# Optimization experiments

Hardware: AMD Instinct MI355X
Metric: run time of the kernel (lower is better)

The kernel has to match this reference:

```python
import jax, jax.numpy as jnp
import numpy as np

D_MODEL = 256
N_LEVELS = 4
N_HEADS = 8
N_POINTS = 4
LEN_Q = 1024
LEN_X = 256
SHAPES_NP = np.array([[100, 100], [50, 50], [25, 25], [13, 13]], dtype=np.int32)
LEN_IN = int((SHAPES_NP[:, 0] * SHAPES_NP[:, 1]).sum())  # 13294


def setup_inputs() -> dict:
    key = jax.random.key(0)
    ks = jax.random.split(key, 10)
    s = 0.02
    lvl_start = np.concatenate([[0], np.cumsum(SHAPES_NP[:, 0] * SHAPES_NP[:, 1])[:-1]]).astype(np.int32)
    return {
        "query": jax.random.normal(ks[0], (1, LEN_Q, D_MODEL), jnp.float32),
        "reference_points": jax.random.uniform(ks[1], (1, LEN_Q, N_LEVELS, 2), jnp.float32),
        "input_flatten": jax.random.normal(ks[2], (1, LEN_IN, D_MODEL), jnp.float32),
        "input_spatial_shapes": jnp.asarray(SHAPES_NP, jnp.int32),
        "add_keys": jax.random.normal(ks[3], (1, LEN_X, D_MODEL), jnp.float32),
        "input_level_start_index": jnp.asarray(lvl_start, jnp.int32),
        "W_off": jax.random.normal(ks[4], (N_HEADS * N_LEVELS * N_POINTS * 2, D_MODEL), jnp.float32) * s,
        "b_off": jax.random.normal(ks[5], (N_HEADS * N_LEVELS * N_POINTS * 2,), jnp.float32),
        "W_attn": jax.random.normal(ks[6], (N_HEADS * (N_LEVELS + 1), D_MODEL, D_MODEL), jnp.float32) * s,
        "W_val": jax.random.normal(ks[7], (2 * N_HEADS, D_MODEL, D_MODEL), jnp.float32) * s,
        "b_val": jax.random.normal(ks[8], (2 * N_HEADS, D_MODEL), jnp.float32) * s,
        "W_mix": jax.random.normal(ks[9], (D_MODEL, N_HEADS + 1), jnp.float32) * s,
    }


def reference(query, reference_points, input_flatten, input_spatial_shapes, add_keys,
              input_level_start_index, W_off, b_off, W_attn, W_val, b_val, W_mix):
    N, Lq, C = query.shape
    H, L, P = N_HEADS, N_LEVELS, N_POINTS

    # sampling offsets: (N, Lq, H, L, P, 2)
    off = (query @ W_off.T + b_off).reshape(N, Lq, H, L, P, 2)
    iss_f = input_spatial_shapes.astype(jnp.float32)          # (L, 2) = (H_l, W_l)
    wh = iss_f[:, ::-1]                                        # (W_l, H_l)
    loc = reference_points[:, :, None, :, None, :] + off / wh[None, None, None, :, None, :]

    # get_keys: clamp, quantize to int index (matches torch .int() trunc, values >= 0)
    loc = jnp.clip(loc, 0.0, 0.999)
    idx = (loc * iss_f[None, None, None, :, None, :]).astype(jnp.int32)
    h_l = input_spatial_shapes[:, 0]                           # (L,)
    flat_idx = (idx[..., 0] + idx[..., 1] * h_l[None, None, None, :, None]
                + input_level_start_index[None, None, None, :, None])   # (N, Lq, H, L, P)
    keys = input_flatten[0][flat_idx[0]]                       # (Lq, H, L, P, C)
    keys = jnp.transpose(keys, (1, 2, 3, 0, 4))                # (H, L, P, Lq, C)

    q = query.reshape(Lq, C)
    head_w = jax.nn.softmax(W_mix.T, axis=0)                   # (H+1, C), softmax over heads
    result = q * head_w[-1][None]
    addk = add_keys.reshape(-1, C)                             # (Lx, C)

    for h in range(H):
        attn = []
        for lvl in range(L):
            simil = W_attn[h * L + lvl]
            # faithful to torch: (C, P*Lq) row-major reshaped to (P, Lq, C)
            ki = (simil @ keys[h, lvl].reshape(-1, C).T).reshape(P, Lq, C)
            attn.append((ki * q[None]).sum(-1))                # (P, Lq)
        simil = W_attn[h * L + L]
        ki = addk @ simil.T                                    # (Lx, C)
        attn.append(ki @ q.T)                                  # (Lx, Lq)
        attn = jax.nn.softmax(jnp.concatenate(attn, axis=0), axis=0)  # (L*P+Lx, Lq)

        vals = (keys[h].reshape(-1, C) @ W_val[2 * h].T + b_val[2 * h]).reshape(L * P, Lq, C)
        v2 = addk @ W_val[2 * h + 1].T + b_val[2 * h + 1]      # (Lx, C)
        vals = jnp.concatenate([vals, jnp.broadcast_to(v2[:, None], (v2.shape[0], Lq, C))], axis=0)
        result = result + (attn[:, :, None] * vals).sum(0) * head_w[h][None]

    return result[None]
```

## Files before the change

### kernel.cpp

```cpp
#include <hip/hip_runtime.h>

typedef unsigned short ushort_t;
typedef __attribute__((ext_vector_type(8))) short bh8;
typedef __attribute__((ext_vector_type(4))) float f4;
typedef __attribute__((ext_vector_type(4))) unsigned int u4;

__device__ __forceinline__ ushort_t f2bf(float f) {
  unsigned u = __float_as_uint(f);
  return (ushort_t)((u + 0x7FFFu + ((u >> 16) & 1u)) >> 16);
}
__device__ __forceinline__ float bf2f(ushort_t v) {
  return __uint_as_float(((unsigned)v) << 16);
}

template <typename OutT>
__device__ __forceinline__ void gemm_abt_core(
    char* smem,
    const ushort_t* __restrict__ A, const ushort_t* __restrict__ B,
    OutT* __restrict__ C, int ldA, int ldB, int ldC, int K, int m0, int n0)
{
  ushort_t* As = (ushort_t*)smem;
  ushort_t* Bs = (ushort_t*)(smem + 10240);
  int t = threadIdx.x;
  int lane = t & 63, w = t >> 6;
  int quad = lane >> 4, l15 = lane & 15;
  int wm = w >> 1, wn = w & 1;
  f4 acc[4][4];
  #pragma unroll
  for (int mi = 0; mi < 4; ++mi)
    #pragma unroll
    for (int ni = 0; ni < 4; ++ni) acc[mi][ni] = (f4)0.f;
  int row = t >> 1, kh = (t & 1) * 16;
  const ushort_t* pa = A + (m0 + row) * ldA + kh;
  const ushort_t* pb = B + (n0 + row) * ldB + kh;
  u4 va0 = *(const u4*)(pa);     u4 va1 = *(const u4*)(pa + 8);
  u4 vb0 = *(const u4*)(pb);     u4 vb1 = *(const u4*)(pb + 8);
  for (int k0 = 0; k0 < K; k0 += 32) {
    if (k0) __syncthreads();
    {
      u4* da = (u4*)(As + row * 40 + kh); da[0] = va0; da[1] = va1;
      u4* db = (u4*)(Bs + row * 40 + kh); db[0] = vb0; db[1] = vb1;
    }
    if (k0 + 32 < K) {
      va0 = *(const u4*)(pa + k0 + 32); va1 = *(const u4*)(pa + k0 + 40);
      vb0 = *(const u4*)(pb + k0 + 32); vb1 = *(const u4*)(pb + k0 + 40);
    }
    __syncthreads();
    bh8 af[4], bfv[4];
    #pragma unroll
    for (int mi = 0; mi < 4; ++mi)
      af[mi] = *(bh8*)(As + (wm * 64 + mi * 16 + l15) * 40 + quad * 8);
    #pragma unroll
    for (int ni = 0; ni < 4; ++ni)
      bfv[ni] = *(bh8*)(Bs + (wn * 64 + ni * 16 + l15) * 40 + quad * 8);
    #pragma unroll
    for (int mi = 0; mi < 4; ++mi)
      #pragma unroll
      for (int ni = 0; ni < 4; ++ni)
        acc[mi][ni] = __builtin_amdgcn_mfma_f32_16x16x32_bf16(af[mi], bfv[ni], acc[mi][ni], 0, 0, 0);
  }
  #pragma unroll
  for (int mi = 0; mi < 4; ++mi)
    #pragma unroll
    for (int ni = 0; ni < 4; ++ni)
      #pragma unroll
      for (int r = 0; r < 4; ++r) {
        int mg = m0 + wm * 64 + mi * 16 + quad * 4 + r;
        int ng = n0 + wn * 64 + ni * 16 + l15;
        if constexpr (sizeof(OutT) == 4) C[mg * ldC + ng] = acc[mi][ni][r];
        else C[mg * ldC + ng] = (OutT)f2bf(acc[mi][ni][r]);
      }
}

__device__ __forceinline__ void gemm_abt_12864(
    char* smem,
    const ushort_t* __restrict__ A, const ushort_t* __restrict__ B,
    float* __restrict__ C, int ldA, int ldB, int ldC, int K, int m0, int n0)
{
  ushort_t* As = (ushort_t*)smem;
  ushort_t* Bs = (ushort_t*)(smem + 10240);
  int t = threadIdx.x;
  int lane = t & 63, w = t >> 6;
  int quad = lane >> 4, l15 = lane & 15;
  int wm = w >> 1, wn = w & 1;
  f4 acc[4][2];
  #pragma unroll
  for (int mi = 0; mi < 4; ++mi)
    #pragma unroll
    for (int ni = 0; ni < 2; ++ni) acc[mi][ni] = (f4)0.f;
  int rowA = t >> 1, khA = (t & 1) * 16;
  int rowB = t >> 2, khB = (t & 3) * 8;
  const ushort_t* pa = A + (m0 + rowA) * ldA + khA;
  const ushort_t* pb = B + (n0 + rowB) * ldB + khB;
  u4 va0 = *(const u4*)(pa); u4 va1 = *(const u4*)(pa + 8);
  u4 vb0 = *(const u4*)(pb);
  for (int k0 = 0; k0 < K; k0 += 32) {
    if (k0) __syncthreads();
    {
      u4* da = (u4*)(As + rowA * 40 + khA); da[0] = va0; da[1] = va1;
      u4* db = (u4*)(Bs + rowB * 40 + khB); db[0] = vb0;
    }
    if (k0 + 32 < K) {
      va0 = *(const u4*)(pa + k0 + 32); va1 = *(const u4*)(pa + k0 + 40);
      vb0 = *(const u4*)(pb + k0 + 32);
    }
    __syncthreads();
    bh8 af[4], bf2[2];
    #pragma unroll
    for (int mi = 0; mi < 4; ++mi)
      af[mi] = *(bh8*)(As + (wm * 64 + mi * 16 + l15) * 40 + quad * 8);
    #pragma unroll
    for (int ni = 0; ni < 2; ++ni)
      bf2[ni] = *(bh8*)(Bs + (wn * 32 + ni * 16 + l15) * 40 + quad * 8);
    #pragma unroll
    for (int mi = 0; mi < 4; ++mi)
      #pragma unroll
      for (int ni = 0; ni < 2; ++ni)
        acc[mi][ni] = __builtin_amdgcn_mfma_f32_16x16x32_bf16(af[mi], bf2[ni], acc[mi][ni], 0, 0, 0);
  }
  #pragma unroll
  for (int mi = 0; mi < 4; ++mi)
    #pragma unroll
    for (int ni = 0; ni < 2; ++ni)
      #pragma unroll
      for (int r = 0; r < 4; ++r) {
        int mg = m0 + wm * 64 + mi * 16 + quad * 4 + r;
        int ng = n0 + wn * 32 + ni * 16 + l15;
        C[mg * ldC + ng] = acc[mi][ni][r];
      }
}

__device__ __forceinline__ void gemm_abt_f32in(
    char* smem,
    const float* __restrict__ A, const float* __restrict__ B,
    ushort_t* __restrict__ C, int ldA, int ldB, int ldC, int K, int m0, int n0)
{
  ushort_t* As = (ushort_t*)smem;
  ushort_t* Bs = (ushort_t*)(smem + 10240);
  int t = threadIdx.x;
  int lane = t & 63, w = t >> 6;
  int quad = lane >> 4, l15 = lane & 15;
  int wm = w >> 1, wn = w & 1;
  f4 acc[4][4];
  #pragma unroll
  for (int mi = 0; mi < 4; ++mi)
    #pragma unroll
    for (int ni = 0; ni < 4; ++ni) acc[mi][ni] = (f4)0.f;
  int row = t >> 1, kh = (t & 1) * 16;
  const float* pa = A + (m0 + row) * ldA + kh;
  const float* pb = B + (n0 + row) * ldB + kh;
  float4 fa[4], fb[4];
  #pragma unroll
  for (int i = 0; i < 4; ++i) {
    fa[i] = *(const float4*)(pa + i * 4);
    fb[i] = *(const float4*)(pb + i * 4);
  }
  for (int k0 = 0; k0 < K; k0 += 32) {
    if (k0) __syncthreads();
    {
      ushort_t* da = As + row * 40 + kh;
      ushort_t* db = Bs + row * 40 + kh;
      #pragma unroll
      for (int i = 0; i < 4; ++i) {
        ushort4 oa; oa.x = f2bf(fa[i].x); oa.y = f2bf(fa[i].y);
        oa.z = f2bf(fa[i].z); oa.w = f2bf(fa[i].w);
        *(ushort4*)(da + i * 4) = oa;
        ushort4 ob; ob.x = f2bf(fb[i].x); ob.y = f2bf(fb[i].y);
        ob.z = f2bf(fb[i].z); ob.w = f2bf(fb[i].w);
        *(ushort4*)(db + i * 4) = ob;
      }
    }
    if (k0 + 32 < K) {
      #pragma unroll
      for (int i = 0; i < 4; ++i) {
        fa[i] = *(const float4*)(pa + k0 + 32 + i * 4);
        fb[i] = *(const float4*)(pb + k0 + 32 + i * 4);
      }
    }
    __syncthreads();
    bh8 af[4], bfv[4];
    #pragma unroll
    for (int mi = 0; mi < 4; ++mi)
      af[mi] = *(bh8*)(As + (wm * 64 + mi * 16 + l15) * 40 + quad * 8);
    #pragma unroll
    for (int ni = 0; ni < 4; ++ni)
      bfv[ni] = *(bh8*)(Bs + (wn * 64 + ni * 16 + l15) * 40 + quad * 8);
    #pragma unroll
    for (int mi = 0; mi < 4; ++mi)
      #pragma unroll
      for (int ni = 0; ni < 4; ++ni)
        acc[mi][ni] = __builtin_amdgcn_mfma_f32_16x16x32_bf16(af[mi], bfv[ni], acc[mi][ni], 0, 0, 0);
  }
  #pragma unroll
  for (int mi = 0; mi < 4; ++mi)
    #pragma unroll
    for (int ni = 0; ni < 4; ++ni)
      #pragma unroll
      for (int r = 0; r < 4; ++r) {
        int mg = m0 + wm * 64 + mi * 16 + quad * 4 + r;
        int ng = n0 + wn * 64 + ni * 16 + l15;
        C[mg * ldC + ng] = (ushort_t)f2bf(acc[mi][ni][r]);
      }
}

__global__ __launch_bounds__(256) void k_fused_cast_off(
    const float* __restrict__ q, const float* __restrict__ xin,
    const float* __restrict__ addk, const float* __restrict__ Wval,
    const float* __restrict__ Wattn, ushort_t* __restrict__ arena,
    const float* __restrict__ Woff, const float* __restrict__ boff,
    const float* __restrict__ refpts, const int* __restrict__ shapes,
    const int* __restrict__ lvlst, int* __restrict__ fidx,
    ushort_t* __restrict__ tmp)
{
  __shared__ __align__(16) char smem[20480];
  if (blockIdx.x >= 96) {
    const int total4 = 1719168;
    for (int i = (blockIdx.x - 96) * 256 + threadIdx.x; i < total4; i += 1952 * 256) {
      const float* src; ushort_t* dst; int e;
      if (i < 65536)        { src = q    + i * 4;            dst = arena + i * 4; }
      else if (i < 916352)  { e = i - 65536;  src = xin  + e * 4; dst = arena + 262144  + e * 4; }
      else if (i < 932736)  { e = i - 916352; src = addk + e * 4; dst = arena + 3665408 + e * 4; }
      else if (i < 1194880) {
        e = i - 932736; int el = e * 4;
        int h = el >> 17, r = el & 131071;
        int c = r >> 9, k = r & 511;
        src = Wval + (2 * h + (k >> 8)) * 65536 + c * 256 + (k & 255);
        dst = arena + 3730944 + el;
      }
      else {
        e = i - 1194880;
        src = Wattn + e * 4;
        dst = arena + 6352384 + e * 4;
      }
      float4 v = *(const float4*)src;
      ushort4 o; o.x = f2bf(v.x); o.y = f2bf(v.y); o.z = f2bf(v.z); o.w = f2bf(v.w);
      *(ushort4*)dst = o;
    }
  } else if (blockIdx.x >= 64) {
    int e = blockIdx.x - 64;
    int h = e >> 2, rem = e & 3, my = rem >> 1, nx = rem & 1;
    gemm_abt_f32in(smem, addk, Wattn + (h * 4 + 4) * 65536, tmp + h * 65536,
                   256, 256, 256, 256, my * 128, nx * 128);
  } else {
    float(*As)[65] = (float(*)[65])smem;
    float(*Bs)[65] = (float(*)[65])(smem + 16 * 65 * 4);
    int e = blockIdx.x;
    int nx = e & 3, my = e >> 2;
    int m0 = my * 64, n0 = nx * 64;
    int t = threadIdx.x;
    int tm = t & 15, tn = t >> 4;
    int lr = t >> 4, lc = t & 15;
    float acc[4][4] = {};
    float qa[4], wb[4];
    #pragma unroll
    for (int i = 0; i < 4; ++i) {
      int r = lr + i * 16;
      qa[i] = q[(m0 + r) * 256 + lc];
      wb[i] = Woff[(n0 + r) * 256 + lc];
    }
    for (int k0 = 0; k0 < 256; k0 += 16) {
      if (k0) __syncthreads();
      #pragma unroll
      for (int i = 0; i < 4; ++i) {
        int r = lr + i * 16;
        As[lc][r] = qa[i];
        Bs[lc][r] = wb[i];
      }
      if (k0 + 16 < 256) {
        #pragma unroll
        for (int i = 0; i < 4; ++i) {
          int r = lr + i * 16;
          qa[i] = q[(m0 + r) * 256 + k0 + 16 + lc];
          wb[i] = Woff[(n0 + r) * 256 + k0 + 16 + lc];
        }
      }
      __syncthreads();
      #pragma unroll
      for (int k = 0; k < 16; ++k) {
        float a[4], b[4];
        #pragma unroll
        for (int i = 0; i < 4; ++i) a[i] = As[k][tm * 4 + i];
        #pragma unroll
        for (int j = 0; j < 4; ++j) b[j] = Bs[k][tn * 4 + j];
        #pragma unroll
        for (int i = 0; i < 4; ++i)
          #pragma unroll
          for (int j = 0; j < 4; ++j) acc[i][j] += a[i] * b[j];
      }
    }
    #pragma unroll
    for (int i = 0; i < 4; ++i) {
      int b = m0 + tm * 4 + i;
      #pragma unroll
      for (int jp = 0; jp < 2; ++jp) {
        int tt = ((n0 + tn * 4) >> 1) + jp;
        int l = (tt >> 2) & 3;
        float off0 = acc[i][jp * 2]     + boff[2 * tt];
        float off1 = acc[i][jp * 2 + 1] + boff[2 * tt + 1];
        int Hi = shapes[2 * l], Wi = shapes[2 * l + 1];
        float Hf = (float)Hi, Wf = (float)Wi;
        float r0 = refpts[b * 8 + 2 * l], r1 = refpts[b * 8 + 2 * l + 1];
        float l0 = fminf(fmaxf(r0 + off0 / Wf, 0.f), 0.999f);
        float l1 = fminf(fmaxf(r1 + off1 / Hf, 0.f), 0.999f);
        int i0 = (int)(l0 * Hf);
        int i1 = (int)(l1 * Wf);
        fidx[b * 128 + tt] = i0 + i1 * Hi + lvlst[l];
      }
    }
  }
}

__device__ __forceinline__ void attn_mfma_body(
    char* smemc,
    const ushort_t* __restrict__ qbf, const ushort_t* __restrict__ xbf,
    const ushort_t* __restrict__ Wlvl, const int* __restrict__ fidx,
    float* __restrict__ attnP, int bx)
{
  unsigned* Bs0 = (unsigned*)smemc;
  unsigned* Bs1 = (unsigned*)(smemc + 8704);
  ushort_t* As0 = (ushort_t*)(smemc + 17408);
  ushort_t* As1 = (ushort_t*)(smemc + 26624);
  int* fis = (int*)(smemc + 35840);
  float* Nlds = (float*)smemc;

  int h = bx >> 8, l = (bx >> 6) & 3, g = bx & 63;
  int ch = g & 3, g2 = g >> 2;
  int p = g2 >> 2, tg = g2 & 3;
  int c0 = ch * 64;
  int t = threadIdx.x;
  int lane = t & 63, w = t >> 6;
  int quad = lane >> 4, l15 = lane & 15;
  int qcol = p * 4 + tg;
  fis[t] = fidx[(tg * 256 + t) * 128 + h * 16 + l * 4 + p];
  __syncthreads();
  f4 acc[4];
  #pragma unroll
  for (int mi = 0; mi < 4; ++mi) acc[mi] = (f4)0.f;

  int cl = t & 63, sg = t >> 6;
  int uu = t >> 2, jj0 = (t & 3) * 16;
  const ushort_t* qrow = qbf + (uu * 16 + qcol) * 256 + jj0;

  unsigned vv[16];
  u4 a0, a1;
  #pragma unroll
  for (int rr = 0; rr < 16; ++rr)
    vv[rr] = xbf[fis[sg * 16 + rr] * 256 + c0 + cl];
  { const u4* src = (const u4*)qrow; a0 = src[0]; a1 = src[1]; }
  #pragma unroll
  for (int i = 0; i < 4; ++i) {
    uint2 w2; w2.x = vv[i * 4] | (vv[i * 4 + 1] << 16);
    w2.y = vv[i * 4 + 2] | (vv[i * 4 + 3] << 16);
    *(uint2*)&Bs0[cl * 34 + sg * 8 + i * 2] = w2;
  }
  { u4* dst = (u4*)(As0 + uu * 72 + jj0); dst[0] = a0; dst[1] = a1; }
  #pragma unroll
  for (int rr = 0; rr < 16; ++rr)
    vv[rr] = xbf[fis[64 + sg * 16 + rr] * 256 + c0 + cl];
  { const u4* src = (const u4*)(qrow + 64); a0 = src[0]; a1 = src[1]; }
  __syncthreads();

  #pragma unroll
  for (int jt = 0; jt < 4; ++jt) {
    unsigned* Bc = (jt & 1) ? Bs1 : Bs0;
    ushort_t* Ac = (jt & 1) ? As1 : As0;
    if (jt < 3) {
      unsigned* Bn = (jt & 1) ? Bs0 : Bs1;
      ushort_t* An = (jt & 1) ? As0 : As1;
      #pragma unroll
      for (int i = 0; i < 4; ++i) {
        uint2 w2; w2.x = vv[i * 4] | (vv[i * 4 + 1] << 16);
        w2.y = vv[i * 4 + 2] | (vv[i * 4 + 3] << 16);
        *(uint2*)&Bn[cl * 34 + sg * 8 + i * 2] = w2;
      }
      { u4* dst = (u4*)(An + uu * 72 + jj0); dst[0] = a0; dst[1] = a1; }
      if (jt < 2) {
        #pragma unroll
        for (int rr = 0; rr < 16; ++rr)
          vv[rr] = xbf[fis[(jt + 2) * 64 + sg * 16 + rr] * 256 + c0 + cl];
        const u4* src = (const u4*)(qrow + (jt + 2) * 64);
        a0 = src[0]; a1 = src[1];
      }
    }
    #pragma unroll
    for (int ks = 0; ks < 2; ++ks) {
      bh8 af[4], bfv;
      #pragma unroll
      for (int mi = 0; mi < 4; ++mi)
        af[mi] = *(bh8*)(Ac + (mi * 16 + l15) * 72 + ks * 32 + quad * 8);
      {
        const unsigned* bp = &Bc[(w * 16 + l15) * 34 + ks * 16 + quad * 4];
        uint2 b0 = *(const uint2*)bp;
        uint2 b1 = *(const uint2*)(bp + 2);
        u4 bb; bb.x = b0.x; bb.y = b0.y; bb.z = b1.x; bb.w = b1.y;
        bfv = __builtin_bit_cast(bh8, bb);
      }
      #pragma unroll
      for (int mi = 0; mi < 4; ++mi)
        acc[mi] = __builtin_amdgcn_mfma_f32_16x16x32_bf16(af[mi], bfv, acc[mi], 0, 0, 0);
    }
    if (jt < 3) __syncthreads();
  }
  __syncthreads();
  #pragma unroll
  for (int mi = 0; mi < 4; ++mi)
    *(f4*)&Nlds[(w * 16 + l15) * 68 + mi * 16 + quad * 4] = acc[mi];
  __syncthreads();
  {
    int a = t >> 6, u = t & 63;
    const ushort_t* Wr = Wlvl + (h * 4 + l) * 65536 + (a * 64 + u) * 256 + c0;
    float s = 0.f;
    #pragma unroll
    for (int cc = 0; cc < 8; ++cc) {
      u4 wv = *(const u4*)(Wr + cc * 8);
      int cb = cc * 8;
      s += __uint_as_float(wv.x << 16)         * Nlds[(cb + 0) * 68 + u];
      s += __uint_as_float(wv.x & 0xffff0000u) * Nlds[(cb + 1) * 68 + u];
      s += __uint_as_float(wv.y << 16)         * Nlds[(cb + 2) * 68 + u];
      s += __uint_as_float(wv.y & 0xffff0000u) * Nlds[(cb + 3) * 68 + u];
      s += __uint_as_float(wv.z << 16)         * Nlds[(cb + 4) * 68 + u];
      s += __uint_as_float(wv.z & 0xffff0000u) * Nlds[(cb + 5) * 68 + u];
      s += __uint_as_float(wv.w << 16)         * Nlds[(cb + 6) * 68 + u];
      s += __uint_as_float(wv.w & 0xffff0000u) * Nlds[(cb + 7) * 68 + u];
    }
    attnP[ch * 131072 + (h * 16 + l * 4 + a) * 1024 + u * 16 + qcol] = s;
  }
}

__global__ __launch_bounds__(256, 4) void k_fused_attn(
    const ushort_t* __restrict__ qbf, const ushort_t* __restrict__ xbf,
    const ushort_t* __restrict__ Wlvl, const int* __restrict__ fidx,
    float* __restrict__ attnP,
    const ushort_t* __restrict__ tmp, float* __restrict__ attn)
{
  __shared__ __align__(16) char smem[36864];
  int bx = blockIdx.x;
  if (bx >= 256) {
    attn_mfma_body(smem, qbf, xbf, Wlvl, fidx, attnP, bx - 256);
  } else {
    int e = bx;
    int h = e >> 5, rem = e & 31, my = rem >> 4, nx = rem & 15;
    gemm_abt_12864(smem, tmp + h * 65536, qbf, attn + h * 278528 + 16384,
                   256, 256, 1024, 256, my * 128, nx * 64);
  }
}

__global__ __launch_bounds__(256) void k_softmax(
    float* __restrict__ attn, const float* __restrict__ attnP,
    ushort_t* __restrict__ attn2bf, float* __restrict__ s1, float* __restrict__ s2)
{
  __shared__ float red[16][17];
  int h = blockIdx.y;
  int bl = threadIdx.x & 15;
  int b = blockIdx.x * 16 + bl;
  int rg = threadIdx.x >> 4;
  const int R0 = rg * 17;
  float* col = attn + h * 278528 + b;
  float v[17];
  float m = -1e30f;
  #pragma unroll
  for (int i = 0; i < 17; ++i) {
    int r = R0 + i;
    float x;
    if (r < 16) {
      int idx = (h * 16 + r) * 1024 + b;
      x = attnP[idx] + attnP[131072 + idx] + attnP[262144 + idx] + attnP[393216 + idx];
    } else {
      x = col[r * 1024];
    }
    v[i] = x;
    m = fmaxf(m, x);
  }
  red[rg][bl] = m;
  __syncthreads();
  #pragma unroll
  for (int j = 0; j < 16; ++j) m = fmaxf(m, red[j][bl]);
  float sum = 0.f;
  #pragma unroll
  for (int i = 0; i < 17; ++i) { v[i] = expf(v[i] - m); sum += v[i]; }
  __syncthreads();
  red[rg][bl] = sum;
  __syncthreads();
  float tot = 0.f;
  #pragma unroll
  for (int j = 0; j < 16; ++j) tot += red[j][bl];
  float inv = 1.f / tot;
  #pragma unroll
  for (int i = 0; i < 17; ++i) {
    int r = R0 + i;
    float x = v[i] * inv;
    if (r < 16) col[r * 1024] = x;
    else attn2bf[h * 262144 + (r - 16) * 1024 + b] = f2bf(x);
  }
  if (rg == 0) {
    float sa = 0.f;
    #pragma unroll
    for (int i = 0; i < 16; ++i) sa += v[i];
    float sn = sa * inv;
    s1[h * 1024 + b] = sn;
    s2[h * 1024 + b] = 1.f - sn;
  }
}

__global__ __launch_bounds__(256) void k_fused_kbar_tn(
    const ushort_t* __restrict__ xbf, const float* __restrict__ attn,
    const int* __restrict__ fidx, const ushort_t* __restrict__ attn2,
    const ushort_t* __restrict__ addk, ushort_t* __restrict__ kabar)
{
  __shared__ __align__(16) unsigned Asu[128 * 20];
  __shared__ __align__(16) unsigned Bsu[128 * 20];
  if (blockIdx.x >= 128) {
    int bb = blockIdx.x - 128;
    int h = bb >> 7, b0 = (bb & 127) * 8;
    int t = threadIdx.x;
    int qi = t >> 5, oct = t & 31;
    int b = b0 + qi;
    float aw[16]; int rowv[16];
    #pragma unroll
    for (int r = 0; r < 16; ++r) {
      aw[r]   = attn[(h * 272 + r) * 1024 + b];
      rowv[r] = fidx[b * 128 + h * 16 + r];
    }
    u4 va[8], vb[8];
    #pragma unroll
    for (int r = 0; r < 8; ++r) va[r] = *(const u4*)(xbf + rowv[r] * 256 + oct * 8);
    #pragma unroll
    for (int r = 0; r < 8; ++r) vb[r] = *(const u4*)(xbf + rowv[8 + r] * 256 + oct * 8);
    float sacc[8] = {};
    #pragma unroll
    for (int r = 0; r < 8; ++r) {
      u4 v = va[r]; float w = aw[r];
      sacc[0] += w * __uint_as_float(v.x << 16);
      sacc[1] += w * __uint_as_float(v.x & 0xffff0000u);
      sacc[2] += w * __uint_as_float(v.y << 16);
      sacc[3] += w * __uint_as_float(v.y & 0xffff0000u);
      sacc[4] += w * __uint_as_float(v.z << 16);
      sacc[5] += w * __uint_as_float(v.z & 0xffff0000u);
      sacc[6] += w * __uint_as_float(v.w << 16);
      sacc[7] += w * __uint_as_float(v.w & 0xffff0000u);
    }
    #pragma unroll
    for (int r = 0; r < 8; ++r) {
      u4 v = vb[r]; float w = aw[8 + r];
      sacc[0] += w * __uint_as_float(v.x << 16);
      sacc[1] += w * __uint_as_float(v.x & 0xffff0000u);
      sacc[2] += w * __uint_as_float(v.y << 16);
      sacc[3] += w * __uint_as_float(v.y & 0xffff0000u);
      sacc[4] += w * __uint_as_float(v.z << 16);
      sacc[5] += w * __uint_as_float(v.z & 0xffff0000u);
      sacc[6] += w * __uint_as_float(v.w << 16);
      sacc[7] += w * __uint_as_float(v.w & 0xffff0000u);
    }
    u4 o;
    o.x = (unsigned)f2bf(sacc[0]) | ((unsigned)f2bf(sacc[1]) << 16);
    o.y = (unsigned)f2bf(sacc[2]) | ((unsigned)f2bf(sacc[3]) << 16);
    o.z = (unsigned)f2bf(sacc[4]) | ((unsigned)f2bf(sacc[5]) << 16);
    o.w = (unsigned)f2bf(sacc[6]) | ((unsigned)f2bf(sacc[7]) << 16);
    *(u4*)(kabar + (h * 1024 + b) * 512 + oct * 8) = o;
  } else {
    int e = blockIdx.x;
    int h = e >> 4, rem = e & 15, my = rem >> 1, nx = rem & 1;
    const ushort_t* A = attn2 + h * 262144;
    const ushort_t* B = addk;
    ushort_t* C = kabar + h * 524288;
    int m0 = my * 128, n0 = nx * 128;
    int t = threadIdx.x;
    int lane = t & 63, w = t >> 6;
    int quad = lane >> 4, l15 = lane & 15;
    int wm = w >> 1, wn = w & 1;
    f4 acc[4][4];
    #pragma unroll
    for (int mi = 0; mi < 4; ++mi)
      #pragma unroll
      for (int ni = 0; ni < 4; ++ni) acc[mi][ni] = (f4)0.f;
    int col = t & 127, half = t >> 7;
    unsigned pa[8], pb[8];
    #pragma unroll
    for (int i = 0; i < 4; ++i) {
      int kpp = half * 4 + i, kk = kpp * 4;
      unsigned x0 = A[(kk + 0) * 1024 + m0 + col], x1 = A[(kk + 1) * 1024 + m0 + col];
      unsigned x2 = A[(kk + 2) * 1024 + m0 + col], x3 = A[(kk + 3) * 1024 + m0 + col];
      pa[i * 2] = x0 | (x1 << 16); pa[i * 2 + 1] = x2 | (x3 << 16);
      unsigned y0 = B[(kk + 0) * 256 + n0 + col], y1 = B[(kk + 1) * 256 + n0 + col];
      unsigned y2 = B[(kk + 2) * 256 + n0 + col], y3 = B[(kk + 3) * 256 + n0 + col];
      pb[i * 2] = y0 | (y1 << 16); pb[i * 2 + 1] = y2 | (y3 << 16);
    }
    for (int k0 = 0; k0 < 256; k0 += 32) {
      if (k0) __syncthreads();
      #pragma unroll
      for (int i = 0; i < 4; ++i) {
        int kpp = half * 4 + i;
        uint2 va; va.x = pa[i * 2]; va.y = pa[i * 2 + 1];
        *(uint2*)&Asu[col * 20 + kpp * 2] = va;
        uint2 vbv; vbv.x = pb[i * 2]; vbv.y = pb[i * 2 + 1];
        *(uint2*)&Bsu[col * 20 + kpp * 2] = vbv;
      }
      if (k0 + 32 < 256) {
        #pragma unroll
        for (int i = 0; i < 4; ++i) {
          int kpp = half * 4 + i, kk = k0 + 32 + kpp * 4;
          unsigned x0 = A[(kk + 0) * 1024 + m0 + col], x1 = A[(kk + 1) * 1024 + m0 + col];
          unsigned x2 = A[(kk + 2) * 1024 + m0 + col], x3 = A[(kk + 3) * 1024 + m0 + col];
          pa[i * 2] = x0 | (x1 << 16); pa[i * 2 + 1] = x2 | (x3 << 16);
          unsigned y0 = B[(kk + 0) * 256 + n0 + col], y1 = B[(kk + 1) * 256 + n0 + col];
          unsigned y2 = B[(kk + 2) * 256 + n0 + col], y3 = B[(kk + 3) * 256 + n0 + col];
          pb[i * 2] = y0 | (y1 << 16); pb[i * 2 + 1] = y2 | (y3 << 16);
        }
      }
      __syncthreads();
      bh8 af[4], bfv[4];
      #pragma unroll
      for (int mi = 0; mi < 4; ++mi)
        af[mi] = *(bh8*)((const ushort_t*)Asu + (wm * 64 + mi * 16 + l15) * 40 + quad * 8);
      #pragma unroll
      for (int ni = 0; ni < 4; ++ni)
        bfv[ni] = *(bh8*)((const ushort_t*)Bsu + (wn * 64 + ni * 16 + l15) * 40 + quad * 8);
      #pragma unroll
      for (int mi = 0; mi < 4; ++mi)
        #pragma unroll
        for (int ni = 0; ni < 4; ++ni)
          acc[mi][ni] = __builtin_amdgcn_mfma_f32_16x16x32_bf16(af[mi], bfv[ni], acc[mi][ni], 0, 0, 0);
    }
    #pragma unroll
    for (int mi = 0; mi < 4; ++mi)
      #pragma unroll
      for (int ni = 0; ni < 4; ++ni)
        #pragma unroll
        for (int r = 0; r < 4; ++r) {
          int mg = m0 + wm * 64 + mi * 16 + quad * 4 + r;
          int ng = n0 + wn * 64 + ni * 16 + l15;
          C[mg * 512 + 256 + ng] = f2bf(acc[mi][ni][r]);
        }
  }
}

__global__ __launch_bounds__(256) void gemm_val_k(
    const ushort_t* __restrict__ kabar, const ushort_t* __restrict__ Wcat,
    float* __restrict__ Y)
{
  __shared__ __align__(16) char smem[20480];
  int h = blockIdx.z;
  gemm_abt_core<float>(smem, kabar + h * 524288, Wcat + h * 131072, Y + h * 262144,
                       512, 512, 256, 512, blockIdx.y * 128, blockIdx.x * 128);
}

__global__ __launch_bounds__(256) void k_combine(
    const float* __restrict__ q, const float* __restrict__ Wmix,
    const float* __restrict__ Y,
    const float* __restrict__ s1, const float* __restrict__ s2,
    const float* __restrict__ bval, float* __restrict__ out)
{
  int b = blockIdx.x, c = threadIdx.x;
  float w[9];
  float m = -1e30f;
  #pragma unroll
  for (int j = 0; j < 9; ++j) { w[j] = Wmix[c * 9 + j]; m = fmaxf(m, w[j]); }
  float tot = 0.f;
  #pragma unroll
  for (int j = 0; j < 9; ++j) { w[j] = expf(w[j] - m); tot += w[j]; }
  float inv = 1.f / tot;
  float res = q[b * 256 + c] * w[8] * inv;
  #pragma unroll
  for (int hh = 0; hh < 8; ++hh) {
    float y = Y[(hh * 1024 + b) * 256 + c]
            + s1[hh * 1024 + b] * bval[(2 * hh) * 256 + c]
            + s2[hh * 1024 + b] * bval[(2 * hh + 1) * 256 + c];
    res += w[hh] * inv * y;
  }
  out[b * 256 + c] = res;
}

extern "C" void kernel_launch(void* const* d_in, const int* in_sizes, int n_in,
                              void* d_out, int out_size, void* d_ws, size_t ws_size,
                              hipStream_t stream) {
  (void)in_sizes; (void)n_in; (void)out_size; (void)ws_size;
  const float* q      = (const float*)d_in[0];
  const float* refpts = (const float*)d_in[1];
  const float* xin    = (const float*)d_in[2];
  const int*   shapes = (const int*)d_in[3];
  const float* addk   = (const float*)d_in[4];
  const int*   lvlst  = (const int*)d_in[5];
  const float* Woff   = (const float*)d_in[6];
  const float* boff   = (const float*)d_in[7];
  const float* Wattn  = (const float*)d_in[8];
  const float* Wval   = (const float*)d_in[9];
  const float* bval   = (const float*)d_in[10];
  const float* Wmix   = (const float*)d_in[11];
  float* out = (float*)d_out;
  float* ws  = (float*)d_ws;

  int*   fidx    = (int*)ws;
  float* s1      = ws + 393216;
  float* s2      = ws + 401408;
  float* attn    = ws + 409600;
  float* Y       = ws + 409600;
  ushort_t* arena = (ushort_t*)(ws + 2637824);
  ushort_t* q_bf     = arena;
  ushort_t* xin_bf   = arena + 262144;
  ushort_t* addk_bf  = arena + 3665408;
  ushort_t* Wcat_bf  = arena + 3730944;
  ushort_t* Wlvl_bf  = arena + 6352384;
  ushort_t* tmp_bf   = arena + 8449536;
  ushort_t* attn2_bf = arena + 8973824;
  ushort_t* kabar_bf = arena + 11070976;
  float* attnP = (float*)(arena + 15265280);

  k_fused_cast_off<<<2048, 256, 0, stream>>>(q, xin, addk, Wval, Wattn, arena,
                                             Woff, boff, refpts, shapes, lvlst,
                                             fidx, tmp_bf);
  k_fused_attn<<<2304, 256, 0, stream>>>(q_bf, xin_bf, Wlvl_bf, fidx, attnP,
                                         tmp_bf, attn);
  k_softmax<<<dim3(64, 8), 256, 0, stream>>>(attn, attnP, attn2_bf, s1, s2);
  k_fused_kbar_tn<<<1152, 256, 0, stream>>>(xin_bf, attn, fidx, attn2_bf,
                                            addk_bf, kabar_bf);
  gemm_val_k<<<dim3(2, 8, 8), 256, 0, stream>>>(kabar_bf, Wcat_bf, Y);
  k_combine<<<1024, 256, 0, stream>>>(q, Wmix, Y, s1, s2, bval, out);
}
```

Measured before the change: 178.0 us.

## Trade register prefetch for occupancy in cast and kbar kernels

Removes the register-held next-tile prefetch from two GEMM paths, loading tiles directly inside each k-step instead. It splits the gather in kbar into two batches of eight loads rather than sixteen, and raises the occupancy hint in launch bounds to 4 blocks per SM. The cast loop is unrolled by two so each thread has two independent loads in flight. The goal is lower register pressure and more resident waves to hide memory latency, at the cost of losing software pipelining of global loads within each block.

```diff
diff --git a/kernel.cpp b/kernel.cpp
--- a/kernel.cpp
+++ b/kernel.cpp
@@ -149,12 +149,6 @@
   int row = t >> 1, kh = (t & 1) * 16;
   const float* pa = A + (m0 + row) * ldA + kh;
   const float* pb = B + (n0 + row) * ldB + kh;
-  float4 fa[4], fb[4];
-  #pragma unroll
-  for (int i = 0; i < 4; ++i) {
-    fa[i] = *(const float4*)(pa + i * 4);
-    fb[i] = *(const float4*)(pb + i * 4);
-  }
   for (int k0 = 0; k0 < K; k0 += 32) {
     if (k0) __syncthreads();
     {
@@ -162,19 +156,14 @@
       ushort_t* db = Bs + row * 40 + kh;
       #pragma unroll
       for (int i = 0; i < 4; ++i) {
-        ushort4 oa; oa.x = f2bf(fa[i].x); oa.y = f2bf(fa[i].y);
-        oa.z = f2bf(fa[i].z); oa.w = f2bf(fa[i].w);
+        float4 fa = *(const float4*)(pa + k0 + i * 4);
+        float4 fb = *(const float4*)(pb + k0 + i * 4);
+        ushort4 oa; oa.x = f2bf(fa.x); oa.y = f2bf(fa.y);
+        oa.z = f2bf(fa.z); oa.w = f2bf(fa.w);
         *(ushort4*)(da + i * 4) = oa;
-        ushort4 ob; ob.x = f2bf(fb[i].x); ob.y = f2bf(fb[i].y);
-        ob.z = f2bf(fb[i].z); ob.w = f2bf(fb[i].w);
+        ushort4 ob; ob.x = f2bf(fb.x); ob.y = f2bf(fb.y);
+        ob.z = f2bf(fb.z); ob.w = f2bf(fb.w);
         *(ushort4*)(db + i * 4) = ob;
-      }
-    }
-    if (k0 + 32 < K) {
-      #pragma unroll
-      for (int i = 0; i < 4; ++i) {
-        fa[i] = *(const float4*)(pa + k0 + 32 + i * 4);
-        fb[i] = *(const float4*)(pb + k0 + 32 + i * 4);
       }
     }
     __syncthreads();
@@ -203,7 +192,32 @@
       }
 }
 
-__global__ __launch_bounds__(256) void k_fused_cast_off(
+__device__ __forceinline__ const float* cast_src(
+    int i, const float* __restrict__ q, const float* __restrict__ xin,
+    const float* __restrict__ addk, const float* __restrict__ Wval,
+    const float* __restrict__ Wattn, ushort_t* __restrict__ arena,
+    ushort_t** dst)
+{
+  const float* src; int e;
+  if (i < 65536)        { src = q    + i * 4;            *dst = arena + i * 4; }
+  else if (i < 916352)  { e = i - 65536;  src = xin  + e * 4; *dst = arena + 262144  + e * 4; }
+  else if (i < 932736)  { e = i - 916352; src = addk + e * 4; *dst = arena + 3665408 + e * 4; }
+  else if (i < 1194880) {
+    e = i - 932736; int el = e * 4;
+    int h = el >> 17, r = el & 131071;
+    int c = r >> 9, k = r & 511;
+    src = Wval + (2 * h + (k >> 8)) * 65536 + c * 256 + (k & 255);
+    *dst = arena + 3730944 + el;
+  }
+  else {
+    e = i - 1194880;
+    src = Wattn + e * 4;
+    *dst = arena + 6352384 + e * 4;
+  }
+  return src;
+}
+
+__global__ __launch_bounds__(256, 4) void k_fused_cast_off(
     const float* __restrict__ q, const float* __restrict__ xin,
     const float* __restrict__ addk, const float* __restrict__ Wval,
     const float* __restrict__ Wattn, ushort_t* __restrict__ arena,
@@ -215,26 +229,22 @@
   __shared__ __align__(16) char smem[20480];
   if (blockIdx.x >= 96) {
     const int total4 = 1719168;
-    for (int i = (blockIdx.x - 96) * 256 + threadIdx.x; i < total4; i += 1952 * 256) {
-      const float* src; ushort_t* dst; int e;
-      if (i < 65536)        { src = q    + i * 4;            dst = arena + i * 4; }
-      else if (i < 916352)  { e = i - 65536;  src = xin  + e * 4; dst = arena + 262144  + e * 4; }
-      else if (i < 932736)  { e = i - 916352; src = addk + e * 4; dst = arena + 3665408 + e * 4; }
-      else if (i < 1194880) {
-        e = i - 932736; int el = e * 4;
-        int h = el >> 17, r = el & 131071;
-        int c = r >> 9, k = r & 511;
-        src = Wval + (2 * h + (k >> 8)) * 65536 + c * 256 + (k & 255);
-        dst = arena + 3730944 + el;
-      }
-      else {
-        e = i - 1194880;
-        src = Wattn + e * 4;
-        dst = arena + 6352384 + e * 4;
-      }
-      float4 v = *(const float4*)src;
-      ushort4 o; o.x = f2bf(v.x); o.y = f2bf(v.y); o.z = f2bf(v.z); o.w = f2bf(v.w);
-      *(ushort4*)dst = o;
+    const int S = 1952 * 256;
+    for (int i = (blockIdx.x - 96) * 256 + threadIdx.x; i < total4; i += 2 * S) {
+      ushort_t* d1; const float* s1 = cast_src(i, q, xin, addk, Wval, Wattn, arena, &d1);
+      float4 v1 = *(const float4*)s1;
+      int i2 = i + S;
+      ushort_t* d2 = nullptr; float4 v2 = v1;
+      if (i2 < total4) {
+        const float* s2 = cast_src(i2, q, xin, addk, Wval, Wattn, arena, &d2);
+        v2 = *(const float4*)s2;
+      }
+      ushort4 o1; o1.x = f2bf(v1.x); o1.y = f2bf(v1.y); o1.z = f2bf(v1.z); o1.w = f2bf(v1.w);
+      *(ushort4*)d1 = o1;
+      if (i2 < total4) {
+        ushort4 o2; o2.x = f2bf(v2.x); o2.y = f2bf(v2.y); o2.z = f2bf(v2.z); o2.w = f2bf(v2.w);
+        *(ushort4*)d2 = o2;
+      }
     }
   } else if (blockIdx.x >= 64) {
     int e = blockIdx.x - 64;
@@ -502,7 +512,7 @@
   }
 }
 
-__global__ __launch_bounds__(256) void k_fused_kbar_tn(
+__global__ __launch_bounds__(256, 4) void k_fused_kbar_tn(
     const ushort_t* __restrict__ xbf, const float* __restrict__ attn,
     const int* __restrict__ fidx, const ushort_t* __restrict__ attn2,
     const ushort_t* __restrict__ addk, ushort_t* __restrict__ kabar)
@@ -521,12 +531,10 @@
       aw[r]   = attn[(h * 272 + r) * 1024 + b];
       rowv[r] = fidx[b * 128 + h * 16 + r];
     }
-    u4 va[8], vb[8];
+    float sacc[8] = {};
+    u4 va[8];
     #pragma unroll
     for (int r = 0; r < 8; ++r) va[r] = *(const u4*)(xbf + rowv[r] * 256 + oct * 8);
-    #pragma unroll
-    for (int r = 0; r < 8; ++r) vb[r] = *(const u4*)(xbf + rowv[8 + r] * 256 + oct * 8);
-    float sacc[8] = {};
     #pragma unroll
     for (int r = 0; r < 8; ++r) {
       u4 v = va[r]; float w = aw[r];
@@ -540,8 +548,10 @@
       sacc[7] += w * __uint_as_float(v.w & 0xffff0000u);
     }
     #pragma unroll
+    for (int r = 0; r < 8; ++r) va[r] = *(const u4*)(xbf + rowv[8 + r] * 256 + oct * 8);
+    #pragma unroll
     for (int r = 0; r < 8; ++r) {
-      u4 v = vb[r]; float w = aw[8 + r];
+      u4 v = va[r]; float w = aw[8 + r];
       sacc[0] += w * __uint_as_float(v.x << 16);
       sacc[1] += w * __uint_as_float(v.x & 0xffff0000u);
       sacc[2] += w * __uint_as_float(v.y << 16);
@@ -574,38 +584,19 @@
       #pragma unroll
       for (int ni = 0; ni < 4; ++ni) acc[mi][ni] = (f4)0.f;
     int col = t & 127, half = t >> 7;
-    unsigned pa[8], pb[8];
-    #pragma unroll
-    for (int i = 0; i < 4; ++i) {
-      int kpp = half * 4 + i, kk = kpp * 4;
-      unsigned x0 = A[(kk + 0) * 1024 + m0 + col], x1 = A[(kk + 1) * 1024 + m0 + col];
-      unsigned x2 = A[(kk + 2) * 1024 + m0 + col], x3 = A[(kk + 3) * 1024 + m0 + col];
-      pa[i * 2] = x0 | (x1 << 16); pa[i * 2 + 1] = x2 | (x3 << 16);
-      unsigned y0 = B[(kk + 0) * 256 + n0 + col], y1 = B[(kk + 1) * 256 + n0 + col];
-      unsigned y2 = B[(kk + 2) * 256 + n0 + col], y3 = B[(kk + 3) * 256 + n0 + col];
-      pb[i * 2] = y0 | (y1 << 16); pb[i * 2 + 1] = y2 | (y3 << 16);
-    }
     for (int k0 = 0; k0 < 256; k0 += 32) {
       if (k0) __syncthreads();
       #pragma unroll
       for (int i = 0; i < 4; ++i) {
-        int kpp = half * 4 + i;
-        uint2 va; va.x = pa[i * 2]; va.y = pa[i * 2 + 1];
+        int kpp = half * 4 + i, kk = k0 + kpp * 4;
+        unsigned x0 = A[(kk + 0) * 1024 + m0 + col], x1 = A[(kk + 1) * 1024 + m0 + col];
+        unsigned x2 = A[(kk + 2) * 1024 + m0 + col], x3 = A[(kk + 3) * 1024 + m0 + col];
+        uint2 va; va.x = x0 | (x1 << 16); va.y = x2 | (x3 << 16);
         *(uint2*)&Asu[col * 20 + kpp * 2] = va;
-        uint2 vbv; vbv.x = pb[i * 2]; vbv.y = pb[i * 2 + 1];
-        *(uint2*)&Bsu[col * 20 + kpp * 2] = vbv;
-      }
-      if (k0 + 32 < 256) {
-        #pragma unroll
-        for (int i = 0; i < 4; ++i) {
-          int kpp = half * 4 + i, kk = k0 + 32 + kpp * 4;
-          unsigned x0 = A[(kk + 0) * 1024 + m0 + col], x1 = A[(kk + 1) * 1024 + m0 + col];
-          unsigned x2 = A[(kk + 2) * 1024 + m0 + col], x3 = A[(kk + 3) * 1024 + m0 + col];
-          pa[i * 2] = x0 | (x1 << 16); pa[i * 2 + 1] = x2 | (x3 << 16);
-          unsigned y0 = B[(kk + 0) * 256 + n0 + col], y1 = B[(kk + 1) * 256 + n0 + col];
-          unsigned y2 = B[(kk + 2) * 256 + n0 + col], y3 = B[(kk + 3) * 256 + n0 + col];
-          pb[i * 2] = y0 | (y1 << 16); pb[i * 2 + 1] = y2 | (y3 << 16);
-        }
+        unsigned y0 = B[(kk + 0) * 256 + n0 + col], y1 = B[(kk + 1) * 256 + n0 + col];
+        unsigned y2 = B[(kk + 2) * 256 + n0 + col], y3 = B[(kk + 3) * 256 + n0 + col];
+        uint2 vb; vb.x = y0 | (y1 << 16); vb.y = y2 | (y3 << 16);
+        *(uint2*)&Bsu[col * 20 + kpp * 2] = vb;
       }
       __syncthreads();
       bh8 af[4], bfv[4];
```

Measured after the change: 205.7 us. +15.6%, slower.
